# Optimization experiments

Hardware: AMD Instinct MI355X
Metric: run time of the kernel (lower is better)

## Reference

```python
import jax, jax.numpy as jnp
import numpy as np

D_X, D_Y, HIDDEN, K = 256, 32, 256, 2
T = 50
SIG_MIN, SIG_MAX = 0.002, 1.0
N = 4096
D_XY = D_X + D_Y
D_IN = D_XY + 2 * HIDDEN  # 800


def setup_inputs() -> dict:
    key = jax.random.key(0)
    ks = jax.random.split(key, 12)
    def w(k, shape, fan):
        return (jax.random.normal(k, shape, jnp.float32) / np.sqrt(fan)).astype(jnp.float32)
    return {
        "xy0": jax.random.normal(ks[0], (N, D_XY), jnp.float32) * SIG_MAX,  # randn * sigma_max * extra_noise(=1)
        "t0": jax.random.randint(ks[1], (N,), 0, K),
        "t_embed": w(ks[2], (K, HIDDEN), 1),
        "tm_w1": w(ks[3], (1, HIDDEN), 1), "tm_b1": jnp.zeros((HIDDEN,), jnp.float32),
        "tm_w2": w(ks[4], (HIDDEN, HIDDEN), HIDDEN), "tm_b2": jnp.zeros((HIDDEN,), jnp.float32),
        "tr_w1": w(ks[5], (D_IN, HIDDEN), D_IN), "tr_b1": jnp.zeros((HIDDEN,), jnp.float32),
        "tr_w2": w(ks[6], (HIDDEN, HIDDEN), HIDDEN), "tr_b2": jnp.zeros((HIDDEN,), jnp.float32),
        "sh_w": w(ks[7], (HIDDEN, D_XY), HIDDEN), "sh_b": jnp.zeros((D_XY,), jnp.float32),
        "ch_w": w(ks[8], (HIDDEN, K), HIDDEN), "ch_b": jnp.zeros((K,), jnp.float32),
    }


def _sigma(t):
    return SIG_MIN * (SIG_MAX / SIG_MIN) ** t


def reference(xy0, t0, t_embed, tm_w1, tm_b1, tm_w2, tm_b2,
              tr_w1, tr_b1, tr_w2, tr_b2, sh_w, sh_b, ch_w, ch_b):
    n = xy0.shape[0]
    silu = jax.nn.silu
    base_key = jax.random.key(42)

    def net(xy, t, tau):
        te = t_embed[t]  # (n, H) embedding lookup
        # time_mlp on scalar tau -> (H,), broadcast over batch (tau is identical per row)
        tm = silu(tau * tm_w1[0] + tm_b1) @ tm_w2 + tm_b2
        tm = jnp.broadcast_to(tm, (n, HIDDEN))
        h = jnp.concatenate([xy, te, tm], axis=-1)  # (n, D_IN)
        h = silu(silu(h @ tr_w1 + tr_b1) @ tr_w2 + tr_b2)
        return h @ sh_w + sh_b, h @ ch_w + ch_b  # score (n, D_XY), logits (n, K)

    def body(carry, t_idx):
        xy, t = carry
        tau = t_idx.astype(jnp.float32) / T
        sig_t = _sigma(tau)
        sig_prev = _sigma((t_idx - 1).astype(jnp.float32) / T)
        step = sig_t ** 2 - sig_prev ** 2  # positive reverse-SDE step size
        score, logits = net(xy, t, tau)
        k1, k2 = jax.random.split(jax.random.fold_in(base_key, t_idx))
        xy = xy + step * score + jnp.sqrt(step) * jax.random.normal(k1, xy.shape, xy.dtype)
        t = jax.random.categorical(k2, logits, axis=-1)  # multinomial(softmax(logits), 1)
        return (xy, t), None

    steps = jnp.arange(T - 1, 0, -1)  # reversed(range(1, T))
    (xy, t), _ = jax.lax.scan(body, (xy0, t0), steps)
    return xy[:, :D_X], xy[:, D_X:], t
```

## Files before the change

kernel.cpp:

```cpp
#include <hip/hip_runtime.h>
#include <math.h>


#define DXY 288
#define HID 256
#define NTHR 512
#define XYP 292
#define HP  260
#define OUT_Y_OFF 1048576
#define OUT_T_OFF 1179648
#define CT_FLOATS (50 * 512)
#define STEP_OFF  CT_FLOATS

typedef unsigned int u32;

__device__ __forceinline__ void tf2x32(u32 k0, u32 k1, u32 x0, u32 x1, u32& o0, u32& o1) {
  u32 ks2 = k0 ^ k1 ^ 0x1BD11BDAu;
#define TFR(r) { x0 += x1; x1 = (x1 << (r)) | (x1 >> (32 - (r))); x1 ^= x0; }
  x0 += k0; x1 += k1;
  TFR(13) TFR(15) TFR(26) TFR(6)
  x0 += k1;  x1 += ks2 + 1u;
  TFR(17) TFR(29) TFR(16) TFR(24)
  x0 += ks2; x1 += k0 + 2u;
  TFR(13) TFR(15) TFR(26) TFR(6)
  x0 += k0;  x1 += k1 + 3u;
  TFR(17) TFR(29) TFR(16) TFR(24)
  x0 += k1;  x1 += ks2 + 4u;
  TFR(13) TFR(15) TFR(26) TFR(6)
  x0 += ks2; x1 += k0 + 5u;
#undef TFR
  o0 = x0; o1 = x1;
}

__device__ __forceinline__ u32 pbits(u32 ka, u32 kb, u32 j) {
  u32 w0, w1;
  tf2x32(ka, kb, 0u, j, w0, w1);
  return w0 ^ w1;
}

__device__ __forceinline__ float u01f(u32 bits) {
  union { u32 i; float f; } v;
  v.i = (bits >> 9) | 0x3F800000u;
  return v.f - 1.0f;
}

__device__ __forceinline__ float erfinv32(float x) {
  float w = -log1pf(-x * x);
  float p;
  if (w < 5.0f) {
    w -= 2.5f;
    p = 2.81022636e-08f;
    p = fmaf(p, w, 3.43273939e-07f);
    p = fmaf(p, w, -3.5233877e-06f);
    p = fmaf(p, w, -4.39150654e-06f);
    p = fmaf(p, w, 0.00021858087f);
    p = fmaf(p, w, -0.00125372503f);
    p = fmaf(p, w, -0.00417768164f);
    p = fmaf(p, w, 0.246640727f);
    p = fmaf(p, w, 1.50140941f);
  } else {
    w = sqrtf(w) - 3.0f;
    p = -0.000200214257f;
    p = fmaf(p, w, 0.000100950558f);
    p = fmaf(p, w, 0.00134934322f);
    p = fmaf(p, w, -0.00367342844f);
    p = fmaf(p, w, 0.00573950773f);
    p = fmaf(p, w, -0.0076224613f);
    p = fmaf(p, w, 0.00943887047f);
    p = fmaf(p, w, 1.00167406f);
    p = fmaf(p, w, 2.83297682f);
  }
  return p * x;
}

__device__ __forceinline__ float nrmf(u32 bits) {
  float val = fmaf(u01f(bits), 2.0f, -0.99999994f);
  return 1.41421356f * erfinv32(val);
}
__device__ __forceinline__ float gumf(u32 bits) {
  float u = fmaxf(u01f(bits), 1.17549435e-38f);
  return -logf(-logf(u));
}
__device__ __forceinline__ float siluf(float x) {
  return x / (1.0f + expf(-x));
}
__device__ __forceinline__ void fma4(float a, const float4& b, float* acc) {
  acc[0] = fmaf(a, b.x, acc[0]);
  acc[1] = fmaf(a, b.y, acc[1]);
  acc[2] = fmaf(a, b.z, acc[2]);
  acc[3] = fmaf(a, b.w, acc[3]);
}

__global__ void precompute_ct(
    const float* __restrict__ t_embed,
    const float* __restrict__ tm_w1, const float* __restrict__ tm_b1,
    const float* __restrict__ tm_w2, const float* __restrict__ tm_b2,
    const float* __restrict__ tr_w1, const float* __restrict__ tr_b1,
    float* __restrict__ ws)
{
  const int t = blockIdx.x + 1;
  const int c = threadIdx.x;
  __shared__ float tmpre[HID];
  __shared__ float tmv[HID];
  const float tau = (float)t / 50.0f;

  tmpre[c] = siluf(fmaf(tau, tm_w1[c], tm_b1[c]));
  __syncthreads();
  {
    float acc = tm_b2[c];
    for (int i = 0; i < HID; i++)
      acc = fmaf(tmpre[i], tm_w2[i * HID + c], acc);
    tmv[c] = acc;
  }
  __syncthreads();
  float D = 0.f;
  for (int i = 0; i < HID; i++)
    D = fmaf(tmv[i], tr_w1[(544 + i) * HID + c], D);
  float ce0 = tr_b1[c], ce1 = tr_b1[c];
  for (int i = 0; i < HID; i++) {
    ce0 = fmaf(t_embed[i], tr_w1[(288 + i) * HID + c], ce0);
    ce1 = fmaf(t_embed[HID + i], tr_w1[(288 + i) * HID + c], ce1);
  }
  ws[t * 512 + c] = ce0 + D;
  ws[t * 512 + 256 + c] = ce1 + D;

  if (c == 0) {
    const double lt = 6.214608098422191;
    float sig_t = (float)(0.002 * exp(((double)t / 50.0) * lt));
    float sig_p = (float)(0.002 * exp(((double)(t - 1) / 50.0) * lt));
    float stepf = sig_t * sig_t - sig_p * sig_p;
    ws[STEP_OFF + 2 * t] = stepf;
    ws[STEP_OFF + 2 * t + 1] = sqrtf(stepf);
  }
}

__global__ __launch_bounds__(NTHR, 2) void sampler_k(
    const float* __restrict__ xy0, const int* __restrict__ t0,
    const float* __restrict__ tr_w1,
    const float* __restrict__ tr_w2, const float* __restrict__ tr_b2,
    const float* __restrict__ sh_w, const float* __restrict__ sh_b,
    const float* __restrict__ ch_w, const float* __restrict__ ch_b,
    const float* __restrict__ ws,
    float* __restrict__ out)
{
  __shared__ float xy_s[16][XYP];
  __shared__ float h1_s[16][HP];
  __shared__ float h2_s[16][HP];
  __shared__ float ct_s[2][HID];
  __shared__ int tcur_s[16];

  const int tid = threadIdx.x;
  const int lane = tid & 63;
  const int w = tid >> 6;
  const int row0g = blockIdx.x * 16;

  const int r0 = lane >> 3;
  const int r1 = r0 + 8;
  const int cg = w * 32 + (lane & 7) * 4;
  const int rE = lane >> 2;
  const int cE = 256 + w * 4 + (lane & 3);

  for (int idx = tid; idx < 16 * (DXY / 4); idx += NTHR) {
    int r = idx / (DXY / 4);
    int q = idx - r * (DXY / 4);
    *(float4*)&xy_s[r][q * 4] = *(const float4*)(xy0 + (row0g + r) * DXY + q * 4);
  }
  if (tid < 16) tcur_s[tid] = t0[row0g + tid];
  ((float*)ct_s)[tid] = ws[49 * 512 + tid];

  float chw0[4], chw1[4];
  #pragma unroll
  for (int j = 0; j < 4; j++) {
    chw0[j] = ch_w[(lane * 4 + j) * 2 + 0];
    chw1[j] = ch_w[(lane * 4 + j) * 2 + 1];
  }
  const float4 b2r = *(const float4*)(tr_b2 + cg);
  const float cb0 = ch_b[0], cb1 = ch_b[1];
  const float4 sbm = *(const float4*)(sh_b + cg);
  const float sbE = sh_b[cE];
  __syncthreads();

  #pragma unroll 1
  for (int t_idx = 49; t_idx >= 1; --t_idx) {
    const float stepf = ws[STEP_OFF + 2 * t_idx];
    const float sstep = ws[STEP_OFF + 2 * t_idx + 1];

    u32 f0, f1, k1a, k1b, k2a, k2b;
    tf2x32(0u, 42u, 0u, (u32)t_idx, f0, f1);
    tf2x32(f0, f1, 0u, 0u, k1a, k1b);
    tf2x32(f0, f1, 0u, 1u, k2a, k2b);

    {
      const int tc0 = tcur_s[r0], tc1 = tcur_s[r1];
      float aA[4] = {0.f, 0.f, 0.f, 0.f};
      float aB[4] = {0.f, 0.f, 0.f, 0.f};
      const float* wp = tr_w1 + cg;
      #pragma unroll 4
      for (int i = 0; i < DXY; i += 4) {
        float4 xA = *(const float4*)&xy_s[r0][i];
        float4 xB = *(const float4*)&xy_s[r1][i];
        float4 b0 = *(const float4*)(wp + (i + 0) * HID);
        float4 b1 = *(const float4*)(wp + (i + 1) * HID);
        float4 b2 = *(const float4*)(wp + (i + 2) * HID);
        float4 b3 = *(const float4*)(wp + (i + 3) * HID);
        fma4(xA.x, b0, aA); fma4(xA.y, b1, aA); fma4(xA.z, b2, aA); fma4(xA.w, b3, aA);
        fma4(xB.x, b0, aB); fma4(xB.y, b1, aB); fma4(xB.z, b2, aB); fma4(xB.w, b3, aB);
      }
      const float4 ctA = *(const float4*)&ct_s[tc0][cg];
      const float4 ctB = *(const float4*)&ct_s[tc1][cg];
      float4 oA, oB;
      oA.x = siluf(aA[0] + ctA.x); oA.y = siluf(aA[1] + ctA.y);
      oA.z = siluf(aA[2] + ctA.z); oA.w = siluf(aA[3] + ctA.w);
      oB.x = siluf(aB[0] + ctB.x); oB.y = siluf(aB[1] + ctB.y);
      oB.z = siluf(aB[2] + ctB.z); oB.w = siluf(aB[3] + ctB.w);
      *(float4*)&h1_s[r0][cg] = oA;
      *(float4*)&h1_s[r1][cg] = oB;
    }
    __syncthreads();

    {
      float aA[4] = {0.f, 0.f, 0.f, 0.f};
      float aB[4] = {0.f, 0.f, 0.f, 0.f};
      const float* wp = tr_w2 + cg;
      #pragma unroll 4
      for (int i = 0; i < HID; i += 4) {
        float4 hA = *(const float4*)&h1_s[r0][i];
        float4 hB = *(const float4*)&h1_s[r1][i];
        float4 b0 = *(const float4*)(wp + (i + 0) * HID);
        float4 b1 = *(const float4*)(wp + (i + 1) * HID);
        float4 b2 = *(const float4*)(wp + (i + 2) * HID);
        float4 b3 = *(const float4*)(wp + (i + 3) * HID);
        fma4(hA.x, b0, aA); fma4(hA.y, b1, aA); fma4(hA.z, b2, aA); fma4(hA.w, b3, aA);
        fma4(hB.x, b0, aB); fma4(hB.y, b1, aB); fma4(hB.z, b2, aB); fma4(hB.w, b3, aB);
      }
      float4 oA, oB;
      oA.x = siluf(aA[0] + b2r.x); oA.y = siluf(aA[1] + b2r.y);
      oA.z = siluf(aA[2] + b2r.z); oA.w = siluf(aA[3] + b2r.w);
      oB.x = siluf(aB[0] + b2r.x); oB.y = siluf(aB[1] + b2r.y);
      oB.z = siluf(aB[2] + b2r.z); oB.w = siluf(aB[3] + b2r.w);
      *(float4*)&h2_s[r0][cg] = oA;
      *(float4*)&h2_s[r1][cg] = oB;
    }
    __syncthreads();

    {
      float4 hL0 = *(const float4*)&h2_s[2 * w][lane * 4];
      float4 hL1 = *(const float4*)&h2_s[2 * w + 1][lane * 4];
      float pA0 = hL0.x * chw0[0] + hL0.y * chw0[1] + hL0.z * chw0[2] + hL0.w * chw0[3];
      float pA1 = hL0.x * chw1[0] + hL0.y * chw1[1] + hL0.z * chw1[2] + hL0.w * chw1[3];
      float pB0 = hL1.x * chw0[0] + hL1.y * chw0[1] + hL1.z * chw0[2] + hL1.w * chw0[3];
      float pB1 = hL1.x * chw1[0] + hL1.y * chw1[1] + hL1.z * chw1[2] + hL1.w * chw1[3];
      #pragma unroll
      for (int off = 32; off > 0; off >>= 1) {
        pA0 += __shfl_xor(pA0, off);
        pA1 += __shfl_xor(pA1, off);
        pB0 += __shfl_xor(pB0, off);
        pB1 += __shfl_xor(pB1, off);
      }
      u32 grow = (u32)(row0g + 2 * w + ((lane >> 1) & 1));
      float g = gumf(pbits(k2a, k2b, grow * 2u + (u32)(lane & 1)));
      float g0 = __shfl(g, 0), g1 = __shfl(g, 1);
      float g2 = __shfl(g, 2), g3 = __shfl(g, 3);
      if (lane == 0) {
        tcur_s[2 * w]     = (pA1 + cb1 + g1 > pA0 + cb0 + g0) ? 1 : 0;
        tcur_s[2 * w + 1] = (pB1 + cb1 + g3 > pB0 + cb0 + g2) ? 1 : 0;
      }
    }

    {
      float sA[4] = {0.f, 0.f, 0.f, 0.f};
      float sB[4] = {0.f, 0.f, 0.f, 0.f};
      const float* wp = sh_w + cg;
      #pragma unroll 4
      for (int i = 0; i < HID; i += 4) {
        float4 hA = *(const float4*)&h2_s[r0][i];
        float4 hB = *(const float4*)&h2_s[r1][i];
        float4 b0 = *(const float4*)(wp + (i + 0) * DXY);
        float4 b1 = *(const float4*)(wp + (i + 1) * DXY);
        float4 b2 = *(const float4*)(wp + (i + 2) * DXY);
        float4 b3 = *(const float4*)(wp + (i + 3) * DXY);
        fma4(hA.x, b0, sA); fma4(hA.y, b1, sA); fma4(hA.z, b2, sA); fma4(hA.w, b3, sA);
        fma4(hB.x, b0, sB); fma4(hB.y, b1, sB); fma4(hB.z, b2, sB); fma4(hB.w, b3, sB);
      }
      const u32 jA = (u32)(row0g + r0) * 288u + (u32)cg;
      const u32 jB = (u32)(row0g + r1) * 288u + (u32)cg;
      float4 xA = *(const float4*)&xy_s[r0][cg];
      float4 xB = *(const float4*)&xy_s[r1][cg];
      xA.x = fmaf(sstep, nrmf(pbits(k1a, k1b, jA + 0u)), fmaf(stepf, sA[0] + sbm.x, xA.x));
      xA.y = fmaf(sstep, nrmf(pbits(k1a, k1b, jA + 1u)), fmaf(stepf, sA[1] + sbm.y, xA.y));
      xA.z = fmaf(sstep, nrmf(pbits(k1a, k1b, jA + 2u)), fmaf(stepf, sA[2] + sbm.z, xA.z));
      xA.w = fmaf(sstep, nrmf(pbits(k1a, k1b, jA + 3u)), fmaf(stepf, sA[3] + sbm.w, xA.w));
      xB.x = fmaf(sstep, nrmf(pbits(k1a, k1b, jB + 0u)), fmaf(stepf, sB[0] + sbm.x, xB.x));
      xB.y = fmaf(sstep, nrmf(pbits(k1a, k1b, jB + 1u)), fmaf(stepf, sB[1] + sbm.y, xB.y));
      xB.z = fmaf(sstep, nrmf(pbits(k1a, k1b, jB + 2u)), fmaf(stepf, sB[2] + sbm.z, xB.z));
      xB.w = fmaf(sstep, nrmf(pbits(k1a, k1b, jB + 3u)), fmaf(stepf, sB[3] + sbm.w, xB.w));
      *(float4*)&xy_s[r0][cg] = xA;
      *(float4*)&xy_s[r1][cg] = xB;
    }

    {
      float sE = 0.f;
      const float* wp = sh_w + cE;
      #pragma unroll 4
      for (int i = 0; i < HID; i += 4) {
        float4 hE = *(const float4*)&h2_s[rE][i];
        const float* bp = wp + i * DXY;
        sE = fmaf(hE.x, bp[0],
             fmaf(hE.y, bp[DXY],
             fmaf(hE.z, bp[2 * DXY],
             fmaf(hE.w, bp[3 * DXY], sE))));
      }
      u32 jE = (u32)(row0g + rE) * 288u + (u32)cE;
      float nE = nrmf(pbits(k1a, k1b, jE));
      xy_s[rE][cE] = fmaf(sstep, nE, fmaf(stepf, sE + sbE, xy_s[rE][cE]));
    }

    if (t_idx > 1) ((float*)ct_s)[tid] = ws[(t_idx - 1) * 512 + tid];
    __syncthreads();
  }

  for (int idx = tid; idx < 16 * 64; idx += NTHR) {
    int r = idx >> 6;
    int c4 = (idx & 63) * 4;
    *(float4*)(out + (row0g + r) * 256 + c4) = *(const float4*)&xy_s[r][c4];
  }
  for (int idx = tid; idx < 16 * 8; idx += NTHR) {
    int r = idx >> 3;
    int c4 = (idx & 7) * 4;
    *(float4*)(out + OUT_Y_OFF + (row0g + r) * 32 + c4) = *(const float4*)&xy_s[r][256 + c4];
  }
  if (tid < 16) out[OUT_T_OFF + row0g + tid] = (float)tcur_s[tid];
}

extern "C" void kernel_launch(void* const* d_in, const int* in_sizes, int n_in,
                              void* d_out, int out_size, void* d_ws, size_t ws_size,
                              hipStream_t stream) {
  (void)in_sizes; (void)n_in; (void)ws_size; (void)out_size;
  const float* xy0     = (const float*)d_in[0];
  const int*   t0      = (const int*)d_in[1];
  const float* t_embed = (const float*)d_in[2];
  const float* tm_w1   = (const float*)d_in[3];
  const float* tm_b1   = (const float*)d_in[4];
  const float* tm_w2   = (const float*)d_in[5];
  const float* tm_b2   = (const float*)d_in[6];
  const float* tr_w1   = (const float*)d_in[7];
  const float* tr_b1   = (const float*)d_in[8];
  const float* tr_w2   = (const float*)d_in[9];
  const float* tr_b2   = (const float*)d_in[10];
  const float* sh_w    = (const float*)d_in[11];
  const float* sh_b    = (const float*)d_in[12];
  const float* ch_w    = (const float*)d_in[13];
  const float* ch_b    = (const float*)d_in[14];
  float* ws  = (float*)d_ws;
  float* out = (float*)d_out;

  precompute_ct<<<49, 256, 0, stream>>>(t_embed, tm_w1, tm_b1, tm_w2, tm_b2,
                                        tr_w1, tr_b1, ws);
  sampler_k<<<256, NTHR, 0, stream>>>(xy0, t0, tr_w1, tr_w2, tr_b2,
                                      sh_w, sh_b, ch_w, ch_b, ws, out);
}
```

Measured before the change: 2.758 ms.

## Transpose weights into workspace and software-pipeline per-thread GEMM loads

Adds a kernel that writes transposed copies of tr_w1, tr_w2 and sh_w into the workspace, so each thread reads contiguous float4 runs along K for its four output columns. The three per-step GEMMs are replaced by a templated routine that double-buffers 8-deep weight and activation loads. Shared-memory row padding is also changed. This costs an extra transpose launch and workspace, and falls back to the old layout if the workspace is too small.

```diff
diff --git a/kernel.cpp b/kernel.cpp
--- a/kernel.cpp
+++ b/kernel.cpp
@@ -5,12 +5,15 @@
 #define DXY 288
 #define HID 256
 #define NTHR 512
-#define XYP 292
-#define HP  260
+#define XYP 296
+#define HP  264
 #define OUT_Y_OFF 1048576
 #define OUT_T_OFF 1179648
-#define CT_FLOATS (50 * 512)
-#define STEP_OFF  CT_FLOATS
+#define STEP_OFF 25600
+#define WS_W1 25728
+#define WS_W2 99584
+#define WS_SW 165248
+#define WS_NEED_BYTES ((size_t)(WS_SW + 73728 + 64) * 4)
 
 typedef unsigned int u32;
 
@@ -84,11 +87,70 @@
 __device__ __forceinline__ float siluf(float x) {
   return x / (1.0f + expf(-x));
 }
-__device__ __forceinline__ void fma4(float a, const float4& b, float* acc) {
-  acc[0] = fmaf(a, b.x, acc[0]);
-  acc[1] = fmaf(a, b.y, acc[1]);
-  acc[2] = fmaf(a, b.z, acc[2]);
-  acc[3] = fmaf(a, b.w, acc[3]);
+
+struct B8 { float4 a0, b0, a1, b1, a2, b2, a3, b3; };
+
+template<bool TR, int LD>
+__device__ __forceinline__ void loadB8(B8& B, const float* p, int kk) {
+  if constexpr (TR) {
+    B.a0 = *(const float4*)(p + 0 * LD + kk); B.b0 = *(const float4*)(p + 0 * LD + kk + 4);
+    B.a1 = *(const float4*)(p + 1 * LD + kk); B.b1 = *(const float4*)(p + 1 * LD + kk + 4);
+    B.a2 = *(const float4*)(p + 2 * LD + kk); B.b2 = *(const float4*)(p + 2 * LD + kk + 4);
+    B.a3 = *(const float4*)(p + 3 * LD + kk); B.b3 = *(const float4*)(p + 3 * LD + kk + 4);
+  } else {
+    B.a0 = *(const float4*)(p + (kk + 0) * LD); B.a1 = *(const float4*)(p + (kk + 1) * LD);
+    B.a2 = *(const float4*)(p + (kk + 2) * LD); B.a3 = *(const float4*)(p + (kk + 3) * LD);
+    B.b0 = *(const float4*)(p + (kk + 4) * LD); B.b1 = *(const float4*)(p + (kk + 5) * LD);
+    B.b2 = *(const float4*)(p + (kk + 6) * LD); B.b3 = *(const float4*)(p + (kk + 7) * LD);
+  }
+}
+
+template<bool TR>
+__device__ __forceinline__ void fma8x4(float acc[4], const float4 x0, const float4 x1, const B8& B) {
+  if constexpr (TR) {
+    acc[0]=fmaf(x0.x,B.a0.x,acc[0]); acc[0]=fmaf(x0.y,B.a0.y,acc[0]); acc[0]=fmaf(x0.z,B.a0.z,acc[0]); acc[0]=fmaf(x0.w,B.a0.w,acc[0]);
+    acc[0]=fmaf(x1.x,B.b0.x,acc[0]); acc[0]=fmaf(x1.y,B.b0.y,acc[0]); acc[0]=fmaf(x1.z,B.b0.z,acc[0]); acc[0]=fmaf(x1.w,B.b0.w,acc[0]);
+    acc[1]=fmaf(x0.x,B.a1.x,acc[1]); acc[1]=fmaf(x0.y,B.a1.y,acc[1]); acc[1]=fmaf(x0.z,B.a1.z,acc[1]); acc[1]=fmaf(x0.w,B.a1.w,acc[1]);
+    acc[1]=fmaf(x1.x,B.b1.x,acc[1]); acc[1]=fmaf(x1.y,B.b1.y,acc[1]); acc[1]=fmaf(x1.z,B.b1.z,acc[1]); acc[1]=fmaf(x1.w,B.b1.w,acc[1]);
+    acc[2]=fmaf(x0.x,B.a2.x,acc[2]); acc[2]=fmaf(x0.y,B.a2.y,acc[2]); acc[2]=fmaf(x0.z,B.a2.z,acc[2]); acc[2]=fmaf(x0.w,B.a2.w,acc[2]);
+    acc[2]=fmaf(x1.x,B.b2.x,acc[2]); acc[2]=fmaf(x1.y,B.b2.y,acc[2]); acc[2]=fmaf(x1.z,B.b2.z,acc[2]); acc[2]=fmaf(x1.w,B.b2.w,acc[2]);
+    acc[3]=fmaf(x0.x,B.a3.x,acc[3]); acc[3]=fmaf(x0.y,B.a3.y,acc[3]); acc[3]=fmaf(x0.z,B.a3.z,acc[3]); acc[3]=fmaf(x0.w,B.a3.w,acc[3]);
+    acc[3]=fmaf(x1.x,B.b3.x,acc[3]); acc[3]=fmaf(x1.y,B.b3.y,acc[3]); acc[3]=fmaf(x1.z,B.b3.z,acc[3]); acc[3]=fmaf(x1.w,B.b3.w,acc[3]);
+  } else {
+    acc[0]=fmaf(x0.x,B.a0.x,acc[0]); acc[1]=fmaf(x0.x,B.a0.y,acc[1]); acc[2]=fmaf(x0.x,B.a0.z,acc[2]); acc[3]=fmaf(x0.x,B.a0.w,acc[3]);
+    acc[0]=fmaf(x0.y,B.a1.x,acc[0]); acc[1]=fmaf(x0.y,B.a1.y,acc[1]); acc[2]=fmaf(x0.y,B.a1.z,acc[2]); acc[3]=fmaf(x0.y,B.a1.w,acc[3]);
+    acc[0]=fmaf(x0.z,B.a2.x,acc[0]); acc[1]=fmaf(x0.z,B.a2.y,acc[1]); acc[2]=fmaf(x0.z,B.a2.z,acc[2]); acc[3]=fmaf(x0.z,B.a2.w,acc[3]);
+    acc[0]=fmaf(x0.w,B.a3.x,acc[0]); acc[1]=fmaf(x0.w,B.a3.y,acc[1]); acc[2]=fmaf(x0.w,B.a3.z,acc[2]); acc[3]=fmaf(x0.w,B.a3.w,acc[3]);
+    acc[0]=fmaf(x1.x,B.b0.x,acc[0]); acc[1]=fmaf(x1.x,B.b0.y,acc[1]); acc[2]=fmaf(x1.x,B.b0.z,acc[2]); acc[3]=fmaf(x1.x,B.b0.w,acc[3]);
+    acc[0]=fmaf(x1.y,B.b1.x,acc[0]); acc[1]=fmaf(x1.y,B.b1.y,acc[1]); acc[2]=fmaf(x1.y,B.b1.z,acc[2]); acc[3]=fmaf(x1.y,B.b1.w,acc[3]);
+    acc[0]=fmaf(x1.z,B.b2.x,acc[0]); acc[1]=fmaf(x1.z,B.b2.y,acc[1]); acc[2]=fmaf(x1.z,B.b2.z,acc[2]); acc[3]=fmaf(x1.z,B.b2.w,acc[3]);
+    acc[0]=fmaf(x1.w,B.b3.x,acc[0]); acc[1]=fmaf(x1.w,B.b3.y,acc[1]); acc[2]=fmaf(x1.w,B.b3.z,acc[2]); acc[3]=fmaf(x1.w,B.b3.w,acc[3]);
+  }
+}
+
+template<bool TR, int LD, int K>
+__device__ __forceinline__ void gemm2(float accA[4], float accB[4],
+                                      const float* bp, const float* aA, const float* aB) {
+  B8 Bp, Bq;
+  float4 xA0 = *(const float4*)(aA),     xA1 = *(const float4*)(aA + 4);
+  float4 xB0 = *(const float4*)(aB),     xB1 = *(const float4*)(aB + 4);
+  loadB8<TR, LD>(Bp, bp, 0);
+  #pragma unroll 2
+  for (int j = 0; j < K / 16; ++j) {
+    const int k1 = j * 16 + 8;
+    const int k2t = j * 16 + 16;
+    const int k2 = (TR || k2t < K) ? k2t : 0;
+    loadB8<TR, LD>(Bq, bp, k1);
+    float4 yA0 = *(const float4*)(aA + k1), yA1 = *(const float4*)(aA + k1 + 4);
+    float4 yB0 = *(const float4*)(aB + k1), yB1 = *(const float4*)(aB + k1 + 4);
+    fma8x4<TR>(accA, xA0, xA1, Bp);
+    fma8x4<TR>(accB, xB0, xB1, Bp);
+    loadB8<TR, LD>(Bp, bp, k2);
+    xA0 = *(const float4*)(aA + k2); xA1 = *(const float4*)(aA + k2 + 4);
+    xB0 = *(const float4*)(aB + k2); xB1 = *(const float4*)(aB + k2 + 4);
+    fma8x4<TR>(accA, yA0, yA1, Bq);
+    fma8x4<TR>(accB, yB0, yB1, Bq);
+  }
 }
 
 __global__ void precompute_ct(
@@ -134,6 +196,25 @@
   }
 }
 
+__global__ void transpose_w(const float* __restrict__ w1, const float* __restrict__ w2,
+                            const float* __restrict__ sw, float* __restrict__ ws)
+{
+  int i = blockIdx.x * 256 + threadIdx.x;
+  if (i < 73728) {
+    int c = i / 288, k = i - c * 288;
+    ws[WS_W1 + i] = w1[k * HID + c];
+  } else if (i < 139264) {
+    int j = i - 73728;
+    int c = j >> 8, k = j & 255;
+    ws[WS_W2 + j] = w2[(k << 8) + c];
+  } else if (i < 212992) {
+    int m = i - 139264;
+    int c = m >> 8, k = m & 255;
+    ws[WS_SW + m] = sw[k * DXY + c];
+  }
+}
+
+template<bool TR>
 __global__ __launch_bounds__(NTHR, 2) void sampler_k(
     const float* __restrict__ xy0, const int* __restrict__ t0,
     const float* __restrict__ tr_w1,
@@ -160,6 +241,11 @@
   const int rE = lane >> 2;
   const int cE = 256 + w * 4 + (lane & 3);
 
+  const float* w1b = TR ? (ws + WS_W1 + cg * 288) : (tr_w1 + cg);
+  const float* w2b = TR ? (ws + WS_W2 + cg * 256) : (tr_w2 + cg);
+  const float* swb = TR ? (ws + WS_SW + cg * 256) : (sh_w + cg);
+  const float* epb = TR ? (ws + WS_SW + cE * 256) : (sh_w + cE);
+
   for (int idx = tid; idx < 16 * (DXY / 4); idx += NTHR) {
     int r = idx / (DXY / 4);
     int q = idx - r * (DXY / 4);
@@ -192,52 +278,30 @@
 
     {
       const int tc0 = tcur_s[r0], tc1 = tcur_s[r1];
-      float aA[4] = {0.f, 0.f, 0.f, 0.f};
-      float aB[4] = {0.f, 0.f, 0.f, 0.f};
-      const float* wp = tr_w1 + cg;
-      #pragma unroll 4
-      for (int i = 0; i < DXY; i += 4) {
-        float4 xA = *(const float4*)&xy_s[r0][i];
-        float4 xB = *(const float4*)&xy_s[r1][i];
-        float4 b0 = *(const float4*)(wp + (i + 0) * HID);
-        float4 b1 = *(const float4*)(wp + (i + 1) * HID);
-        float4 b2 = *(const float4*)(wp + (i + 2) * HID);
-        float4 b3 = *(const float4*)(wp + (i + 3) * HID);
-        fma4(xA.x, b0, aA); fma4(xA.y, b1, aA); fma4(xA.z, b2, aA); fma4(xA.w, b3, aA);
-        fma4(xB.x, b0, aB); fma4(xB.y, b1, aB); fma4(xB.z, b2, aB); fma4(xB.w, b3, aB);
-      }
+      float accA[4] = {0.f, 0.f, 0.f, 0.f};
+      float accB[4] = {0.f, 0.f, 0.f, 0.f};
+      gemm2<TR, TR ? 288 : HID, 288>(accA, accB, w1b, &xy_s[r0][0], &xy_s[r1][0]);
       const float4 ctA = *(const float4*)&ct_s[tc0][cg];
       const float4 ctB = *(const float4*)&ct_s[tc1][cg];
       float4 oA, oB;
-      oA.x = siluf(aA[0] + ctA.x); oA.y = siluf(aA[1] + ctA.y);
-      oA.z = siluf(aA[2] + ctA.z); oA.w = siluf(aA[3] + ctA.w);
-      oB.x = siluf(aB[0] + ctB.x); oB.y = siluf(aB[1] + ctB.y);
-      oB.z = siluf(aB[2] + ctB.z); oB.w = siluf(aB[3] + ctB.w);
+      oA.x = siluf(accA[0] + ctA.x); oA.y = siluf(accA[1] + ctA.y);
+      oA.z = siluf(accA[2] + ctA.z); oA.w = siluf(accA[3] + ctA.w);
+      oB.x = siluf(accB[0] + ctB.x); oB.y = siluf(accB[1] + ctB.y);
+      oB.z = siluf(accB[2] + ctB.z); oB.w = siluf(accB[3] + ctB.w);
       *(float4*)&h1_s[r0][cg] = oA;
       *(float4*)&h1_s[r1][cg] = oB;
     }
     __syncthreads();
 
     {
-      float aA[4] = {0.f, 0.f, 0.f, 0.f};
-      float aB[4] = {0.f, 0.f, 0.f, 0.f};
-      const float* wp = tr_w2 + cg;
-      #pragma unroll 4
-      for (int i = 0; i < HID; i += 4) {
-        float4 hA = *(const float4*)&h1_s[r0][i];
-        float4 hB = *(const float4*)&h1_s[r1][i];
-        float4 b0 = *(const float4*)(wp + (i + 0) * HID);
-        float4 b1 = *(const float4*)(wp + (i + 1) * HID);
-        float4 b2 = *(const float4*)(wp + (i + 2) * HID);
-        float4 b3 = *(const float4*)(wp + (i + 3) * HID);
-        fma4(hA.x, b0, aA); fma4(hA.y, b1, aA); fma4(hA.z, b2, aA); fma4(hA.w, b3, aA);
-        fma4(hB.x, b0, aB); fma4(hB.y, b1, aB); fma4(hB.z, b2, aB); fma4(hB.w, b3, aB);
-      }
+      float accA[4] = {0.f, 0.f, 0.f, 0.f};
+      float accB[4] = {0.f, 0.f, 0.f, 0.f};
+      gemm2<TR, TR ? 256 : HID, 256>(accA, accB, w2b, &h1_s[r0][0], &h1_s[r1][0]);
       float4 oA, oB;
-      oA.x = siluf(aA[0] + b2r.x); oA.y = siluf(aA[1] + b2r.y);
-      oA.z = siluf(aA[2] + b2r.z); oA.w = siluf(aA[3] + b2r.w);
-      oB.x = siluf(aB[0] + b2r.x); oB.y = siluf(aB[1] + b2r.y);
-      oB.z = siluf(aB[2] + b2r.z); oB.w = siluf(aB[3] + b2r.w);
+      oA.x = siluf(accA[0] + b2r.x); oA.y = siluf(accA[1] + b2r.y);
+      oA.z = siluf(accA[2] + b2r.z); oA.w = siluf(accA[3] + b2r.w);
+      oB.x = siluf(accB[0] + b2r.x); oB.y = siluf(accB[1] + b2r.y);
+      oB.z = siluf(accB[2] + b2r.z); oB.w = siluf(accB[3] + b2r.w);
       *(float4*)&h2_s[r0][cg] = oA;
       *(float4*)&h2_s[r1][cg] = oB;
     }
@@ -268,48 +332,43 @@
     }
 
     {
-      float sA[4] = {0.f, 0.f, 0.f, 0.f};
-      float sB[4] = {0.f, 0.f, 0.f, 0.f};
-      const float* wp = sh_w + cg;
-      #pragma unroll 4
-      for (int i = 0; i < HID; i += 4) {
-        float4 hA = *(const float4*)&h2_s[r0][i];
-        float4 hB = *(const float4*)&h2_s[r1][i];
-        float4 b0 = *(const float4*)(wp + (i + 0) * DXY);
-        float4 b1 = *(const float4*)(wp + (i + 1) * DXY);
-        float4 b2 = *(const float4*)(wp + (i + 2) * DXY);
-        float4 b3 = *(const float4*)(wp + (i + 3) * DXY);
-        fma4(hA.x, b0, sA); fma4(hA.y, b1, sA); fma4(hA.z, b2, sA); fma4(hA.w, b3, sA);
-        fma4(hB.x, b0, sB); fma4(hB.y, b1, sB); fma4(hB.z, b2, sB); fma4(hB.w, b3, sB);
-      }
+      float accA[4] = {0.f, 0.f, 0.f, 0.f};
+      float accB[4] = {0.f, 0.f, 0.f, 0.f};
+      gemm2<TR, TR ? 256 : DXY, 256>(accA, accB, swb, &h2_s[r0][0], &h2_s[r1][0]);
       const u32 jA = (u32)(row0g + r0) * 288u + (u32)cg;
       const u32 jB = (u32)(row0g + r1) * 288u + (u32)cg;
       float4 xA = *(const float4*)&xy_s[r0][cg];
       float4 xB = *(const float4*)&xy_s[r1][cg];
-      xA.x = fmaf(sstep, nrmf(pbits(k1a, k1b, jA + 0u)), fmaf(stepf, sA[0] + sbm.x, xA.x));
-      xA.y = fmaf(sstep, nrmf(pbits(k1a, k1b, jA + 1u)), fmaf(stepf, sA[1] + sbm.y, xA.y));
-      xA.z = fmaf(sstep, nrmf(pbits(k1a, k1b, jA + 2u)), fmaf(stepf, sA[2] + sbm.z, xA.z));
-      xA.w = fmaf(sstep, nrmf(pbits(k1a, k1b, jA + 3u)), fmaf(stepf, sA[3] + sbm.w, xA.w));
-      xB.x = fmaf(sstep, nrmf(pbits(k1a, k1b, jB + 0u)), fmaf(stepf, sB[0] + sbm.x, xB.x));
-      xB.y = fmaf(sstep, nrmf(pbits(k1a, k1b, jB + 1u)), fmaf(stepf, sB[1] + sbm.y, xB.y));
-      xB.z = fmaf(sstep, nrmf(pbits(k1a, k1b, jB + 2u)), fmaf(stepf, sB[2] + sbm.z, xB.z));
-      xB.w = fmaf(sstep, nrmf(pbits(k1a, k1b, jB + 3u)), fmaf(stepf, sB[3] + sbm.w, xB.w));
+      xA.x = fmaf(sstep, nrmf(pbits(k1a, k1b, jA + 0u)), fmaf(stepf, accA[0] + sbm.x, xA.x));
+      xA.y = fmaf(sstep, nrmf(pbits(k1a, k1b, jA + 1u)), fmaf(stepf, accA[1] + sbm.y, xA.y));
+      xA.z = fmaf(sstep, nrmf(pbits(k1a, k1b, jA + 2u)), fmaf(stepf, accA[2] + sbm.z, xA.z));
+      xA.w = fmaf(sstep, nrmf(pbits(k1a, k1b, jA + 3u)), fmaf(stepf, accA[3] + sbm.w, xA.w));
+      xB.x = fmaf(sstep, nrmf(pbits(k1a, k1b, jB + 0u)), fmaf(stepf, accB[0] + sbm.x, xB.x));
+      xB.y = fmaf(sstep, nrmf(pbits(k1a, k1b, jB + 1u)), fmaf(stepf, accB[1] + sbm.y, xB.y));
+      xB.z = fmaf(sstep, nrmf(pbits(k1a, k1b, jB + 2u)), fmaf(stepf, accB[2] + sbm.z, xB.z));
+      xB.w = fmaf(sstep, nrmf(pbits(k1a, k1b, jB + 3u)), fmaf(stepf, accB[3] + sbm.w, xB.w));
       *(float4*)&xy_s[r0][cg] = xA;
       *(float4*)&xy_s[r1][cg] = xB;
     }
 
     {
-      float sE = 0.f;
-      const float* wp = sh_w + cE;
+      float sE0 = 0.f, sE1 = 0.f;
       #pragma unroll 4
-      for (int i = 0; i < HID; i += 4) {
-        float4 hE = *(const float4*)&h2_s[rE][i];
-        const float* bp = wp + i * DXY;
-        sE = fmaf(hE.x, bp[0],
-             fmaf(hE.y, bp[DXY],
-             fmaf(hE.z, bp[2 * DXY],
-             fmaf(hE.w, bp[3 * DXY], sE))));
+      for (int k = 0; k < 256; k += 8) {
+        float4 h0  = *(const float4*)&h2_s[rE][k];
+        float4 h1v = *(const float4*)&h2_s[rE][k + 4];
+        if constexpr (TR) {
+          float4 wa = *(const float4*)(epb + k);
+          float4 wb = *(const float4*)(epb + k + 4);
+          sE0 = fmaf(h0.w, wa.w, fmaf(h0.z, wa.z, fmaf(h0.y, wa.y, fmaf(h0.x, wa.x, sE0))));
+          sE1 = fmaf(h1v.w, wb.w, fmaf(h1v.z, wb.z, fmaf(h1v.y, wb.y, fmaf(h1v.x, wb.x, sE1))));
+        } else {
+          const float* bp2 = epb + k * DXY;
+          sE0 = fmaf(h0.w, bp2[3 * DXY], fmaf(h0.z, bp2[2 * DXY], fmaf(h0.y, bp2[DXY], fmaf(h0.x, bp2[0], sE0))));
+          sE1 = fmaf(h1v.w, bp2[7 * DXY], fmaf(h1v.z, bp2[6 * DXY], fmaf(h1v.y, bp2[5 * DXY], fmaf(h1v.x, bp2[4 * DXY], sE1))));
+        }
       }
+      float sE = sE0 + sE1;
       u32 jE = (u32)(row0g + rE) * 288u + (u32)cE;
       float nE = nrmf(pbits(k1a, k1b, jE));
       xy_s[rE][cE] = fmaf(sstep, nE, fmaf(stepf, sE + sbE, xy_s[rE][cE]));
@@ -335,7 +394,7 @@
 extern "C" void kernel_launch(void* const* d_in, const int* in_sizes, int n_in,
                               void* d_out, int out_size, void* d_ws, size_t ws_size,
                               hipStream_t stream) {
-  (void)in_sizes; (void)n_in; (void)ws_size; (void)out_size;
+  (void)in_sizes; (void)n_in; (void)out_size;
   const float* xy0     = (const float*)d_in[0];
   const int*   t0      = (const int*)d_in[1];
   const float* t_embed = (const float*)d_in[2];
@@ -356,6 +415,12 @@
 
   precompute_ct<<<49, 256, 0, stream>>>(t_embed, tm_w1, tm_b1, tm_w2, tm_b2,
                                         tr_w1, tr_b1, ws);
-  sampler_k<<<256, NTHR, 0, stream>>>(xy0, t0, tr_w1, tr_w2, tr_b2,
-                                      sh_w, sh_b, ch_w, ch_b, ws, out);
-}
+  if (ws_size >= WS_NEED_BYTES) {
+    transpose_w<<<832, 256, 0, stream>>>(tr_w1, tr_w2, sh_w, ws);
+    sampler_k<true><<<256, NTHR, 0, stream>>>(xy0, t0, tr_w1, tr_w2, tr_b2,
+                                              sh_w, sh_b, ch_w, ch_b, ws, out);
+  } else {
+    sampler_k<false><<<256, NTHR, 0, stream>>>(xy0, t0, tr_w1, tr_w2, tr_b2,
+                                               sh_w, sh_b, ch_w, ch_b, ws, out);
+  }
+}
```

Result: slower. 9.298 ms (+237.1%).

## Double threads per block, narrow per-thread tile to 2 columns with prefetched GEMM

Applied to the files above, without the earlier changes.

Raises the block to 1024 threads (16 waves), so each thread computes a 2x2 output tile (two rows, two columns) instead of 2x4. The three per-step GEMMs now share a templated routine that software-pipelines the weight loads with double-buffered register sets. Shared-memory row padding changes, categorical sampling goes to one row per wave, and the extra score columns use two accumulators. Latency hiding should improve, at the cost of fewer FMAs per weight load and register pressure under launch_bounds(1024,4).

```diff
diff --git a/kernel.cpp b/kernel.cpp
--- a/kernel.cpp
+++ b/kernel.cpp
@@ -4,13 +4,12 @@
 
 #define DXY 288
 #define HID 256
-#define NTHR 512
-#define XYP 292
-#define HP  260
+#define NTHR 1024
+#define XYP 296
+#define HP  264
 #define OUT_Y_OFF 1048576
 #define OUT_T_OFF 1179648
-#define CT_FLOATS (50 * 512)
-#define STEP_OFF  CT_FLOATS
+#define STEP_OFF 25600
 
 typedef unsigned int u32;
 
@@ -84,11 +83,64 @@
 __device__ __forceinline__ float siluf(float x) {
   return x / (1.0f + expf(-x));
 }
-__device__ __forceinline__ void fma4(float a, const float4& b, float* acc) {
-  acc[0] = fmaf(a, b.x, acc[0]);
-  acc[1] = fmaf(a, b.y, acc[1]);
-  acc[2] = fmaf(a, b.z, acc[2]);
-  acc[3] = fmaf(a, b.w, acc[3]);
+
+struct Bf2 { float2 r0, r1, r2, r3, r4, r5, r6, r7; };
+
+template<int LD>
+__device__ __forceinline__ void loadBf2(Bf2& B, const float* p, int kk) {
+  const float* q = p + kk * LD;
+  B.r0 = *(const float2*)(q);
+  B.r1 = *(const float2*)(q + LD);
+  B.r2 = *(const float2*)(q + 2 * LD);
+  B.r3 = *(const float2*)(q + 3 * LD);
+  B.r4 = *(const float2*)(q + 4 * LD);
+  B.r5 = *(const float2*)(q + 5 * LD);
+  B.r6 = *(const float2*)(q + 6 * LD);
+  B.r7 = *(const float2*)(q + 7 * LD);
+}
+
+__device__ __forceinline__ void fmaBf2(float acc[4], const float4 a0, const float4 a1,
+                                       const float4 b0, const float4 b1, const Bf2& B) {
+  acc[0]=fmaf(a0.x,B.r0.x,acc[0]); acc[1]=fmaf(a0.x,B.r0.y,acc[1]);
+  acc[2]=fmaf(b0.x,B.r0.x,acc[2]); acc[3]=fmaf(b0.x,B.r0.y,acc[3]);
+  acc[0]=fmaf(a0.y,B.r1.x,acc[0]); acc[1]=fmaf(a0.y,B.r1.y,acc[1]);
+  acc[2]=fmaf(b0.y,B.r1.x,acc[2]); acc[3]=fmaf(b0.y,B.r1.y,acc[3]);
+  acc[0]=fmaf(a0.z,B.r2.x,acc[0]); acc[1]=fmaf(a0.z,B.r2.y,acc[1]);
+  acc[2]=fmaf(b0.z,B.r2.x,acc[2]); acc[3]=fmaf(b0.z,B.r2.y,acc[3]);
+  acc[0]=fmaf(a0.w,B.r3.x,acc[0]); acc[1]=fmaf(a0.w,B.r3.y,acc[1]);
+  acc[2]=fmaf(b0.w,B.r3.x,acc[2]); acc[3]=fmaf(b0.w,B.r3.y,acc[3]);
+  acc[0]=fmaf(a1.x,B.r4.x,acc[0]); acc[1]=fmaf(a1.x,B.r4.y,acc[1]);
+  acc[2]=fmaf(b1.x,B.r4.x,acc[2]); acc[3]=fmaf(b1.x,B.r4.y,acc[3]);
+  acc[0]=fmaf(a1.y,B.r5.x,acc[0]); acc[1]=fmaf(a1.y,B.r5.y,acc[1]);
+  acc[2]=fmaf(b1.y,B.r5.x,acc[2]); acc[3]=fmaf(b1.y,B.r5.y,acc[3]);
+  acc[0]=fmaf(a1.z,B.r6.x,acc[0]); acc[1]=fmaf(a1.z,B.r6.y,acc[1]);
+  acc[2]=fmaf(b1.z,B.r6.x,acc[2]); acc[3]=fmaf(b1.z,B.r6.y,acc[3]);
+  acc[0]=fmaf(a1.w,B.r7.x,acc[0]); acc[1]=fmaf(a1.w,B.r7.y,acc[1]);
+  acc[2]=fmaf(b1.w,B.r7.x,acc[2]); acc[3]=fmaf(b1.w,B.r7.y,acc[3]);
+}
+
+template<int LD, int K>
+__device__ __forceinline__ void gemmf2(float acc[4], const float* wp,
+                                       const float* aA, const float* aB) {
+  constexpr int n = K / 8;
+  Bf2 Bp, Bq;
+  float4 xA0, xA1, xB0, xB1, yA0, yA1, yB0, yB1;
+  loadBf2<LD>(Bp, wp, 0);
+  xA0 = *(const float4*)(aA);     xA1 = *(const float4*)(aA + 4);
+  xB0 = *(const float4*)(aB);     xB1 = *(const float4*)(aB + 4);
+  #pragma unroll 2
+  for (int j = 0; j < n; j += 2) {
+    const int k1 = (j + 1) * 8;
+    loadBf2<LD>(Bq, wp, k1);
+    yA0 = *(const float4*)(aA + k1); yA1 = *(const float4*)(aA + k1 + 4);
+    yB0 = *(const float4*)(aB + k1); yB1 = *(const float4*)(aB + k1 + 4);
+    fmaBf2(acc, xA0, xA1, xB0, xB1, Bp);
+    const int k2 = (j + 2 < n) ? (j + 2) * 8 : 0;
+    loadBf2<LD>(Bp, wp, k2);
+    xA0 = *(const float4*)(aA + k2); xA1 = *(const float4*)(aA + k2 + 4);
+    xB0 = *(const float4*)(aB + k2); xB1 = *(const float4*)(aB + k2 + 4);
+    fmaBf2(acc, yA0, yA1, yB0, yB1, Bq);
+  }
 }
 
 __global__ void precompute_ct(
@@ -134,7 +186,7 @@
   }
 }
 
-__global__ __launch_bounds__(NTHR, 2) void sampler_k(
+__global__ __launch_bounds__(NTHR, 4) void sampler_k(
     const float* __restrict__ xy0, const int* __restrict__ t0,
     const float* __restrict__ tr_w1,
     const float* __restrict__ tr_w2, const float* __restrict__ tr_b2,
@@ -156,9 +208,14 @@
 
   const int r0 = lane >> 3;
   const int r1 = r0 + 8;
-  const int cg = w * 32 + (lane & 7) * 4;
+  const int cg = w * 16 + (lane & 7) * 2;
   const int rE = lane >> 2;
-  const int cE = 256 + w * 4 + (lane & 3);
+  const int cE = 256 + (w & 7) * 4 + (lane & 3);
+
+  const float* w1b = tr_w1 + cg;
+  const float* w2b = tr_w2 + cg;
+  const float* swb = sh_w + cg;
+  const float* epb = sh_w + cE;
 
   for (int idx = tid; idx < 16 * (DXY / 4); idx += NTHR) {
     int r = idx / (DXY / 4);
@@ -166,7 +223,7 @@
     *(float4*)&xy_s[r][q * 4] = *(const float4*)(xy0 + (row0g + r) * DXY + q * 4);
   }
   if (tid < 16) tcur_s[tid] = t0[row0g + tid];
-  ((float*)ct_s)[tid] = ws[49 * 512 + tid];
+  if (tid < 512) ((float*)ct_s)[tid] = ws[49 * 512 + tid];
 
   float chw0[4], chw1[4];
   #pragma unroll
@@ -174,9 +231,9 @@
     chw0[j] = ch_w[(lane * 4 + j) * 2 + 0];
     chw1[j] = ch_w[(lane * 4 + j) * 2 + 1];
   }
-  const float4 b2r = *(const float4*)(tr_b2 + cg);
+  const float2 b2r = *(const float2*)(tr_b2 + cg);
   const float cb0 = ch_b[0], cb1 = ch_b[1];
-  const float4 sbm = *(const float4*)(sh_b + cg);
+  const float2 sbm = *(const float2*)(sh_b + cg);
   const float sbE = sh_b[cE];
   __syncthreads();
 
@@ -192,141 +249,87 @@
 
     {
       const int tc0 = tcur_s[r0], tc1 = tcur_s[r1];
-      float aA[4] = {0.f, 0.f, 0.f, 0.f};
-      float aB[4] = {0.f, 0.f, 0.f, 0.f};
-      const float* wp = tr_w1 + cg;
-      #pragma unroll 4
-      for (int i = 0; i < DXY; i += 4) {
-        float4 xA = *(const float4*)&xy_s[r0][i];
-        float4 xB = *(const float4*)&xy_s[r1][i];
-        float4 b0 = *(const float4*)(wp + (i + 0) * HID);
-        float4 b1 = *(const float4*)(wp + (i + 1) * HID);
-        float4 b2 = *(const float4*)(wp + (i + 2) * HID);
-        float4 b3 = *(const float4*)(wp + (i + 3) * HID);
-        fma4(xA.x, b0, aA); fma4(xA.y, b1, aA); fma4(xA.z, b2, aA); fma4(xA.w, b3, aA);
-        fma4(xB.x, b0, aB); fma4(xB.y, b1, aB); fma4(xB.z, b2, aB); fma4(xB.w, b3, aB);
-      }
-      const float4 ctA = *(const float4*)&ct_s[tc0][cg];
-      const float4 ctB = *(const float4*)&ct_s[tc1][cg];
-      float4 oA, oB;
-      oA.x = siluf(aA[0] + ctA.x); oA.y = siluf(aA[1] + ctA.y);
-      oA.z = siluf(aA[2] + ctA.z); oA.w = siluf(aA[3] + ctA.w);
-      oB.x = siluf(aB[0] + ctB.x); oB.y = siluf(aB[1] + ctB.y);
-      oB.z = siluf(aB[2] + ctB.z); oB.w = siluf(aB[3] + ctB.w);
-      *(float4*)&h1_s[r0][cg] = oA;
-      *(float4*)&h1_s[r1][cg] = oB;
+      float acc[4] = {0.f, 0.f, 0.f, 0.f};
+      gemmf2<HID, 288>(acc, w1b, &xy_s[r0][0], &xy_s[r1][0]);
+      const float2 ctA = *(const float2*)&ct_s[tc0][cg];
+      const float2 ctB = *(const float2*)&ct_s[tc1][cg];
+      float2 oA, oB;
+      oA.x = siluf(acc[0] + ctA.x); oA.y = siluf(acc[1] + ctA.y);
+      oB.x = siluf(acc[2] + ctB.x); oB.y = siluf(acc[3] + ctB.y);
+      *(float2*)&h1_s[r0][cg] = oA;
+      *(float2*)&h1_s[r1][cg] = oB;
     }
     __syncthreads();
 
     {
-      float aA[4] = {0.f, 0.f, 0.f, 0.f};
-      float aB[4] = {0.f, 0.f, 0.f, 0.f};
-      const float* wp = tr_w2 + cg;
-      #pragma unroll 4
-      for (int i = 0; i < HID; i += 4) {
-        float4 hA = *(const float4*)&h1_s[r0][i];
-        float4 hB = *(const float4*)&h1_s[r1][i];
-        float4 b0 = *(const float4*)(wp + (i + 0) * HID);
-        float4 b1 = *(const float4*)(wp + (i + 1) * HID);
-        float4 b2 = *(const float4*)(wp + (i + 2) * HID);
-        float4 b3 = *(const float4*)(wp + (i + 3) * HID);
-        fma4(hA.x, b0, aA); fma4(hA.y, b1, aA); fma4(hA.z, b2, aA); fma4(hA.w, b3, aA);
-        fma4(hB.x, b0, aB); fma4(hB.y, b1, aB); fma4(hB.z, b2, aB); fma4(hB.w, b3, aB);
-      }
-      float4 oA, oB;
-      oA.x = siluf(aA[0] + b2r.x); oA.y = siluf(aA[1] + b2r.y);
-      oA.z = siluf(aA[2] + b2r.z); oA.w = siluf(aA[3] + b2r.w);
-      oB.x = siluf(aB[0] + b2r.x); oB.y = siluf(aB[1] + b2r.y);
-      oB.z = siluf(aB[2] + b2r.z); oB.w = siluf(aB[3] + b2r.w);
-      *(float4*)&h2_s[r0][cg] = oA;
-      *(float4*)&h2_s[r1][cg] = oB;
+      float acc[4] = {0.f, 0.f, 0.f, 0.f};
+      gemmf2<HID, 256>(acc, w2b, &h1_s[r0][0], &h1_s[r1][0]);
+      float2 oA, oB;
+      oA.x = siluf(acc[0] + b2r.x); oA.y = siluf(acc[1] + b2r.y);
+      oB.x = siluf(acc[2] + b2r.x); oB.y = siluf(acc[3] + b2r.y);
+      *(float2*)&h2_s[r0][cg] = oA;
+      *(float2*)&h2_s[r1][cg] = oB;
     }
     __syncthreads();
 
     {
-      float4 hL0 = *(const float4*)&h2_s[2 * w][lane * 4];
-      float4 hL1 = *(const float4*)&h2_s[2 * w + 1][lane * 4];
-      float pA0 = hL0.x * chw0[0] + hL0.y * chw0[1] + hL0.z * chw0[2] + hL0.w * chw0[3];
-      float pA1 = hL0.x * chw1[0] + hL0.y * chw1[1] + hL0.z * chw1[2] + hL0.w * chw1[3];
-      float pB0 = hL1.x * chw0[0] + hL1.y * chw0[1] + hL1.z * chw0[2] + hL1.w * chw0[3];
-      float pB1 = hL1.x * chw1[0] + hL1.y * chw1[1] + hL1.z * chw1[2] + hL1.w * chw1[3];
+      float4 hL = *(const float4*)&h2_s[w][lane * 4];
+      float p0 = hL.x * chw0[0] + hL.y * chw0[1] + hL.z * chw0[2] + hL.w * chw0[3];
+      float p1 = hL.x * chw1[0] + hL.y * chw1[1] + hL.z * chw1[2] + hL.w * chw1[3];
       #pragma unroll
       for (int off = 32; off > 0; off >>= 1) {
-        pA0 += __shfl_xor(pA0, off);
-        pA1 += __shfl_xor(pA1, off);
-        pB0 += __shfl_xor(pB0, off);
-        pB1 += __shfl_xor(pB1, off);
+        p0 += __shfl_xor(p0, off);
+        p1 += __shfl_xor(p1, off);
       }
-      u32 grow = (u32)(row0g + 2 * w + ((lane >> 1) & 1));
-      float g = gumf(pbits(k2a, k2b, grow * 2u + (u32)(lane & 1)));
+      float g = gumf(pbits(k2a, k2b, (u32)(row0g + w) * 2u + (u32)(lane & 1)));
       float g0 = __shfl(g, 0), g1 = __shfl(g, 1);
-      float g2 = __shfl(g, 2), g3 = __shfl(g, 3);
-      if (lane == 0) {
-        tcur_s[2 * w]     = (pA1 + cb1 + g1 > pA0 + cb0 + g0) ? 1 : 0;
-        tcur_s[2 * w + 1] = (pB1 + cb1 + g3 > pB0 + cb0 + g2) ? 1 : 0;
-      }
+      if (lane == 0)
+        tcur_s[w] = (p1 + cb1 + g1 > p0 + cb0 + g0) ? 1 : 0;
     }
 
     {
-      float sA[4] = {0.f, 0.f, 0.f, 0.f};
-      float sB[4] = {0.f, 0.f, 0.f, 0.f};
-      const float* wp = sh_w + cg;
-      #pragma unroll 4
-      for (int i = 0; i < HID; i += 4) {
-        float4 hA = *(const float4*)&h2_s[r0][i];
-        float4 hB = *(const float4*)&h2_s[r1][i];
-        float4 b0 = *(const float4*)(wp + (i + 0) * DXY);
-        float4 b1 = *(const float4*)(wp + (i + 1) * DXY);
-        float4 b2 = *(const float4*)(wp + (i + 2) * DXY);
-        float4 b3 = *(const float4*)(wp + (i + 3) * DXY);
-        fma4(hA.x, b0, sA); fma4(hA.y, b1, sA); fma4(hA.z, b2, sA); fma4(hA.w, b3, sA);
-        fma4(hB.x, b0, sB); fma4(hB.y, b1, sB); fma4(hB.z, b2, sB); fma4(hB.w, b3, sB);
-      }
+      float acc[4] = {0.f, 0.f, 0.f, 0.f};
+      gemmf2<DXY, 256>(acc, swb, &h2_s[r0][0], &h2_s[r1][0]);
       const u32 jA = (u32)(row0g + r0) * 288u + (u32)cg;
       const u32 jB = (u32)(row0g + r1) * 288u + (u32)cg;
-      float4 xA = *(const float4*)&xy_s[r0][cg];
-      float4 xB = *(const float4*)&xy_s[r1][cg];
-      xA.x = fmaf(sstep, nrmf(pbits(k1a, k1b, jA + 0u)), fmaf(stepf, sA[0] + sbm.x, xA.x));
-      xA.y = fmaf(sstep, nrmf(pbits(k1a, k1b, jA + 1u)), fmaf(stepf, sA[1] + sbm.y, xA.y));
-      xA.z = fmaf(sstep, nrmf(pbits(k1a, k1b, jA + 2u)), fmaf(stepf, sA[2] + sbm.z, xA.z));
-      xA.w = fmaf(sstep, nrmf(pbits(k1a, k1b, jA + 3u)), fmaf(stepf, sA[3] + sbm.w, xA.w));
-      xB.x = fmaf(sstep, nrmf(pbits(k1a, k1b, jB + 0u)), fmaf(stepf, sB[0] + sbm.x, xB.x));
-      xB.y = fmaf(sstep, nrmf(pbits(k1a, k1b, jB + 1u)), fmaf(stepf, sB[1] + sbm.y, xB.y));
-      xB.z = fmaf(sstep, nrmf(pbits(k1a, k1b, jB + 2u)), fmaf(stepf, sB[2] + sbm.z, xB.z));
-      xB.w = fmaf(sstep, nrmf(pbits(k1a, k1b, jB + 3u)), fmaf(stepf, sB[3] + sbm.w, xB.w));
-      *(float4*)&xy_s[r0][cg] = xA;
-      *(float4*)&xy_s[r1][cg] = xB;
-    }
-
-    {
-      float sE = 0.f;
-      const float* wp = sh_w + cE;
+      float2 xA = *(const float2*)&xy_s[r0][cg];
+      float2 xB = *(const float2*)&xy_s[r1][cg];
+      xA.x = fmaf(sstep, nrmf(pbits(k1a, k1b, jA + 0u)), fmaf(stepf, acc[0] + sbm.x, xA.x));
+      xA.y = fmaf(sstep, nrmf(pbits(k1a, k1b, jA + 1u)), fmaf(stepf, acc[1] + sbm.y, xA.y));
+      xB.x = fmaf(sstep, nrmf(pbits(k1a, k1b, jB + 0u)), fmaf(stepf, acc[2] + sbm.x, xB.x));
+      xB.y = fmaf(sstep, nrmf(pbits(k1a, k1b, jB + 1u)), fmaf(stepf, acc[3] + sbm.y, xB.y));
+      *(float2*)&xy_s[r0][cg] = xA;
+      *(float2*)&xy_s[r1][cg] = xB;
+    }
+
+    if (w < 8) {
+      float sE0 = 0.f, sE1 = 0.f;
       #pragma unroll 4
-      for (int i = 0; i < HID; i += 4) {
-        float4 hE = *(const float4*)&h2_s[rE][i];
-        const float* bp = wp + i * DXY;
-        sE = fmaf(hE.x, bp[0],
-             fmaf(hE.y, bp[DXY],
-             fmaf(hE.z, bp[2 * DXY],
-             fmaf(hE.w, bp[3 * DXY], sE))));
+      for (int k = 0; k < 256; k += 8) {
+        float4 h0  = *(const float4*)&h2_s[rE][k];
+        float4 h1v = *(const float4*)&h2_s[rE][k + 4];
+        const float* bp2 = epb + k * DXY;
+        sE0 = fmaf(h0.w, bp2[3 * DXY], fmaf(h0.z, bp2[2 * DXY], fmaf(h0.y, bp2[DXY], fmaf(h0.x, bp2[0], sE0))));
+        sE1 = fmaf(h1v.w, bp2[7 * DXY], fmaf(h1v.z, bp2[6 * DXY], fmaf(h1v.y, bp2[5 * DXY], fmaf(h1v.x, bp2[4 * DXY], sE1))));
       }
+      float sE = sE0 + sE1;
       u32 jE = (u32)(row0g + rE) * 288u + (u32)cE;
       float nE = nrmf(pbits(k1a, k1b, jE));
       xy_s[rE][cE] = fmaf(sstep, nE, fmaf(stepf, sE + sbE, xy_s[rE][cE]));
     }
 
-    if (t_idx > 1) ((float*)ct_s)[tid] = ws[(t_idx - 1) * 512 + tid];
+    if (t_idx > 1 && tid < 512) ((float*)ct_s)[tid] = ws[(t_idx - 1) * 512 + tid];
     __syncthreads();
   }
 
-  for (int idx = tid; idx < 16 * 64; idx += NTHR) {
-    int r = idx >> 6;
-    int c4 = (idx & 63) * 4;
+  {
+    int r = tid >> 6;
+    int c4 = (tid & 63) * 4;
     *(float4*)(out + (row0g + r) * 256 + c4) = *(const float4*)&xy_s[r][c4];
   }
-  for (int idx = tid; idx < 16 * 8; idx += NTHR) {
-    int r = idx >> 3;
-    int c4 = (idx & 7) * 4;
+  if (tid < 16 * 8) {
+    int r = tid >> 3;
+    int c4 = (tid & 7) * 4;
     *(float4*)(out + OUT_Y_OFF + (row0g + r) * 32 + c4) = *(const float4*)&xy_s[r][256 + c4];
   }
   if (tid < 16) out[OUT_T_OFF + row0g + tid] = (float)tcur_s[tid];
```

Measured after the change: 4.755 ms. 1.72x slower.
